# Optimization experiments

Hardware: AMD Instinct MI355X
Metric: run time of the kernel (lower is better)

Reference implementation:

```python
import jax, jax.numpy as jnp
import numpy as np

B, N, D, H = 4, 256, 32, 512

def setup_inputs() -> dict:
    key = jax.random.key(0)
    ks = jax.random.split(key, 6)
    z = jax.random.normal(ks[0], (B, N, D), dtype=jnp.float32)
    motif_mask = (jax.random.uniform(ks[1], (B, N)) > 0.5).astype(jnp.float32)
    residue_mask = jnp.ones((B, N), dtype=jnp.float32)
    # Linear weights stored as (in, out); scaled like torch default init
    W1 = jax.random.normal(ks[2], (D * D, H), dtype=jnp.float32) / np.sqrt(D * D)
    b1 = jnp.zeros((H,), dtype=jnp.float32)
    W2 = jax.random.normal(ks[3], (H, H // 2), dtype=jnp.float32) / np.sqrt(H)
    b2 = jnp.zeros((H // 2,), dtype=jnp.float32)
    W3 = jax.random.normal(ks[4], (H // 2, 1), dtype=jnp.float32) / np.sqrt(H // 2)
    b3 = jnp.zeros((1,), dtype=jnp.float32)
    return {"z": z, "motif_mask": motif_mask, "residue_mask": residue_mask,
            "W1": W1, "b1": b1, "W2": W2, "b2": b2, "W3": W3, "b3": b3}

def reference(z, motif_mask, residue_mask, W1, b1, W2, b2, W3, b3):
    # kron[b,i,j, a*D+c] = z[b,i,a] * z[b,j,c]; first Linear on kron is the
    # bilinear form z_i^T W1_h z_j -- compute via two matmuls, never
    # materializing the (B,N,N,D^2) tensor.
    d = z.shape[-1]
    W1r = W1.reshape(d, d, -1)                      # (D, D, H); axis0 = z_i dim, axis1 = z_j dim
    tmp = jnp.einsum('bia,ach->bihc', z, W1r)        # (B, N, H, D)
    h1 = jax.nn.relu(jnp.einsum('bihc,bjc->bijh', tmp, z) + b1)  # (B, N, N, H)
    h2 = jax.nn.relu(jnp.einsum('bijh,hk->bijk', h1, W2) + b2)   # (B, N, N, H/2)
    contact_logits = (jnp.einsum('bijk,ko->bijo', h2, W3) + b3)[..., 0]  # (B, N, N)
    outer_mask = motif_mask[:, None, :] * motif_mask[:, :, None]
    contact_logits = contact_logits * outer_mask
    contact_map = jax.nn.sigmoid(contact_logits)
    return (contact_map, contact_logits)
```

## Files before the change

### kernel.cpp

```cpp
#include <hip/hip_runtime.h>
#include <hip/hip_bf16.h>
#include <cstdint>
#include <cstddef>

#define NB 4
#define NN 256
#define DD 32
#define HH 512

typedef __attribute__((ext_vector_type(8))) short short8;
typedef __attribute__((ext_vector_type(4))) float f32x4;
typedef __attribute__((ext_vector_type(16))) float f32x16;

static __device__ __forceinline__ unsigned cvtpk(float a, float b) {
  unsigned r;
  asm("v_cvt_pk_bf16_f32 %0, %1, %2" : "=v"(r) : "v"(a), "v"(b));
  return r;
}
static __device__ __forceinline__ unsigned short f2bf1(float a) {
  return (unsigned short)(cvtpk(a, 0.f) & 0xffffu);
}

static __device__ __forceinline__ short8 pack8(float4 a0, float4 a1) {
  union { unsigned u[4]; short8 s; } r;
  r.u[0] = cvtpk(a0.x, a0.y); r.u[1] = cvtpk(a0.z, a0.w);
  r.u[2] = cvtpk(a1.x, a1.y); r.u[3] = cvtpk(a1.z, a1.w);
  return r.s;
}

__global__ __launch_bounds__(256) void prep0(const float* __restrict__ W1,
                                             unsigned short* __restrict__ W1F) {
  const int f = blockIdx.x * 256 + threadIdx.x;
  #pragma unroll
  for (int r = 0; r < 4; ++r) {
    int row = r * 16384 + f;
    int lane = row & 63;
    int nt = (row >> 6) & 7, w2 = (row >> 9) & 3, nblk = row >> 11;
    int quad = lane >> 4, l16 = lane & 15;
    int nl = w2 * 128 + l16 * 8 + nt;
    int hl = nl >> 5, c = nl & 31;
    const float* src = W1 + (size_t)(nblk * 16 + hl);
    float v[8];
    #pragma unroll
    for (int e = 0; e < 8; ++e)
      v[e] = src[(size_t)((quad * 8 + e) * 32 + c) * 512];
    uint4 p;
    p.x = cvtpk(v[0], v[1]); p.y = cvtpk(v[2], v[3]);
    p.z = cvtpk(v[4], v[5]); p.w = cvtpk(v[6], v[7]);
    *(uint4*)&W1F[(size_t)row * 8] = p;
  }
}

__global__ __launch_bounds__(256) void prep1(const float* __restrict__ z,
                                             const unsigned short* __restrict__ W1F,
                                             const float* __restrict__ W2,
                                             const float* __restrict__ motif,
                                             unsigned short* __restrict__ W2F,
                                             unsigned short* __restrict__ Tall,
                                             int* __restrict__ jlist,
                                             int* __restrict__ jcnt,
                                             int* __restrict__ wq,
                                             int* __restrict__ wqn,
                                             float* __restrict__ out) {
  const int blk = blockIdx.x;
  const int tid = threadIdx.x;
  if (blk < 512) {
    const int nblk = blk >> 4, mgrp = blk & 15;
    const int bibase = mgrp * 64;
    const int w2 = tid >> 6, lane = tid & 63;
    const int quad = lane >> 4, l16 = lane & 15;

    short8 bfr[8];
    #pragma unroll
    for (int nt = 0; nt < 8; ++nt)
      bfr[nt] = *(const short8*)&W1F[(size_t)((((nblk * 4 + w2) * 8) + nt) * 64 + lane) * 8];

    const int ncol = nblk * 512 + w2 * 128 + l16 * 8;
    #pragma unroll
    for (int mtg = 0; mtg < 2; ++mtg) {
      short8 afr[2];
      #pragma unroll
      for (int mi = 0; mi < 2; ++mi) {
        const float* zr = z + (size_t)(bibase + (mtg * 2 + mi) * 16 + l16) * 32 + quad * 8;
        float4 a0 = *(const float4*)(zr);
        float4 a1 = *(const float4*)(zr + 4);
        afr[mi] = pack8(a0, a1);
      }
      f32x4 d[2][8];
      #pragma unroll
      for (int mi = 0; mi < 2; ++mi)
        #pragma unroll
        for (int nt = 0; nt < 8; ++nt)
          d[mi][nt] = __builtin_amdgcn_mfma_f32_16x16x32_bf16(
              afr[mi], bfr[nt], (f32x4){0.f, 0.f, 0.f, 0.f}, 0, 0, 0);
      #pragma unroll
      for (int mi = 0; mi < 2; ++mi)
        #pragma unroll
        for (int r = 0; r < 4; ++r) {
          int rowbi = bibase + (mtg * 2 + mi) * 16 + quad * 4 + r;
          if (motif[rowbi] != 0.f) {
            uint4 p;
            p.x = cvtpk(d[mi][0][r], d[mi][1][r]);
            p.y = cvtpk(d[mi][2][r], d[mi][3][r]);
            p.z = cvtpk(d[mi][4][r], d[mi][5][r]);
            p.w = cvtpk(d[mi][6][r], d[mi][7][r]);
            *(uint4*)&Tall[(size_t)rowbi * 16384 + ncol] = p;
          }
        }
    }
  } else if (blk < 576) {
    int f8 = (blk - 512) * 256 + tid;
    int lane = f8 & 63;
    int nt = (f8 >> 6) & 1, s = (f8 >> 7) & 3, hc = (f8 >> 9) & 7, w = (f8 >> 12) & 3;
    int k2 = w * 64 + nt * 32 + (lane & 31);
    int hb = hc * 64 + s * 16 + (lane >> 5) * 8;
    float v[8];
    #pragma unroll
    for (int e = 0; e < 8; ++e) v[e] = W2[(hb + e) * 256 + k2];
    uint4 p;
    p.x = cvtpk(v[0], v[1]); p.y = cvtpk(v[2], v[3]);
    p.z = cvtpk(v[4], v[5]); p.w = cvtpk(v[6], v[7]);
    ((uint4*)W2F)[f8] = p;
  } else if (blk == 576) {
    __shared__ int itemc[4];
    __shared__ int baseh[4];
    const int w = tid >> 6, lane = tid & 63;
    int cnt = 0;
    if (w < NB) {
      #pragma unroll
      for (int ch = 0; ch < 4; ++ch) {
        int j = ch * 64 + lane;
        float m = motif[w * 256 + j];
        bool alive = (m != 0.f);
        unsigned long long mk = __ballot(alive);
        unsigned long long below = mk & ((1ull << lane) - 1ull);
        int pos = __popcll(below);
        if (alive) jlist[w * 256 + cnt + pos] = j;
        cnt += __popcll(mk);
      }
      if (lane == 0) {
        jcnt[w] = cnt;
        itemc[w] = cnt * ((cnt + 63) >> 6);
      }
    }
    __syncthreads();
    if (tid == 0) {
      int s = 0;
      #pragma unroll
      for (int k = 0; k < NB; ++k) { baseh[k] = s; s += itemc[k]; }
      *wqn = s;
    }
    __syncthreads();
    if (w < NB) {
      const int K = (cnt + 63) >> 6;
      const int base = baseh[w];
      const int L2n = cnt * K;
      int rank = 0;
      #pragma unroll
      for (int ch = 0; ch < 4; ++ch) {
        int i = ch * 64 + lane;
        bool alive = (motif[w * 256 + i] != 0.f);
        unsigned long long mk = __ballot(alive);
        unsigned long long below = mk & ((1ull << lane) - 1ull);
        int pos = __popcll(below);
        if (alive) {
          int idx0 = (rank + pos) * K;
          for (int jt = 0; jt < K; ++jt) {
            int idx = idx0 + jt;
            int nidx = idx;
            if (K == 2) {
              int g = idx >> 4;
              if (g * 16 + 16 <= L2n)
                nidx = g * 16 + ((idx & 1) << 3) + ((idx >> 1) & 7);
            }
            wq[base + nidx] = (w * 256 + i) * 4 + jt;
          }
        }
        rank += __popcll(mk);
      }
    }
  } else {
    const size_t OUT2 = (size_t)NB * NN * NN;
    const int c = blk - 577;
    for (int p = c * 4096 + tid; p < (c + 1) * 4096; p += 256) {
      int bi = p >> 8, j = p & 255, b = bi >> 8;
      if (motif[bi] == 0.f || motif[b * 256 + j] == 0.f) {
        out[p] = 0.5f;
        out[OUT2 + p] = 0.f;
      }
    }
  }
}

__global__ __launch_bounds__(256) void fused(const unsigned short* __restrict__ Tall,
                                             const unsigned short* __restrict__ W2F,
                                             const float* __restrict__ z,
                                             const float* __restrict__ b1,
                                             const float* __restrict__ b2,
                                             const float* __restrict__ W3,
                                             const float* __restrict__ b3,
                                             const float* __restrict__ motif,
                                             const int* __restrict__ jlist,
                                             const int* __restrict__ jcnt,
                                             const int* __restrict__ wq,
                                             const int* __restrict__ wqn,
                                             float* __restrict__ out) {
  __shared__ unsigned short h1s[2][64 * 264];
  __shared__ float red[256];

  const int bx = blockIdx.x;
  const int tid = threadIdx.x;
  const size_t OUT2 = (size_t)NB * NN * NN;
  const int nq = *wqn;

  if (bx >= nq) return;
  const int item = wq[bx];

  const int w = tid >> 6, lane = tid & 63;
  const int quad = lane >> 4, l16 = lane & 15;
  const int L = lane >> 5, c32 = lane & 31;

  const int bi = item >> 2, jt = item & 3;
  const int b = bi >> 8;
  const int cnt = jcnt[b];
  const int slotbase = jt * 64;
  const float mi_v = motif[bi];

  const unsigned short* Tbase = Tall + (size_t)bi * 16384 + (w * 16 + l16) * 32 + quad * 8;
  const unsigned short* Wp = W2F + w * 32768 + lane * 8;
  const float* b1base = b1 + w * 16 + quad * 4;

  short8 bfp[8][2];
  #pragma unroll
  for (int p = 0; p < 8; ++p) {
    bfp[p][0] = *(const short8*)(Wp + p * 1024);
    bfp[p][1] = *(const short8*)(Wp + p * 1024 + 512);
  }

  short8 zfr[4];
  #pragma unroll
  for (int sg = 0; sg < 4; ++sg) {
    int slot = slotbase + sg * 16 + l16;
    int sc = slot < cnt ? slot : cnt - 1;
    int jj = jlist[b * 256 + sc] & 255;
    const float* zr = z + (size_t)(b * 256 + jj) * 32 + quad * 8;
    float4 a0 = *(const float4*)(zr);
    float4 a1 = *(const float4*)(zr + 4);
    zfr[sg] = pack8(a0, a1);
  }

  float b2v[2], w3v[2];
  #pragma unroll
  for (int nt = 0; nt < 2; ++nt) {
    int k2 = w * 64 + nt * 32 + c32;
    b2v[nt] = b2[k2];
    w3v[nt] = W3[k2];
  }

  f32x16 acc[2][2];
  #pragma unroll
  for (int mt = 0; mt < 2; ++mt)
    #pragma unroll
    for (int nt = 0; nt < 2; ++nt)
      acc[mt][nt] = (f32x16){0.f,0.f,0.f,0.f,0.f,0.f,0.f,0.f,
                             0.f,0.f,0.f,0.f,0.f,0.f,0.f,0.f};

  short8 tfr[4];

  #pragma unroll
  for (int q = 0; q < 4; ++q)
    tfr[q] = *(const short8*)(Tbase + q * 2048);
  #pragma unroll
  for (int q = 0; q < 4; ++q) {
    float4 b1f = *(const float4*)(b1base + q * 64);
    f32x4 cin = {b1f.x, b1f.y, b1f.z, b1f.w};
    #pragma unroll
    for (int sg = 0; sg < 4; ++sg) {
      f32x4 d = __builtin_amdgcn_mfma_f32_16x16x32_bf16(tfr[q], zfr[sg], cin, 0, 0, 0);
      uint2 p;
      p.x = cvtpk(fmaxf(d[0], 0.f), fmaxf(d[1], 0.f));
      p.y = cvtpk(fmaxf(d[2], 0.f), fmaxf(d[3], 0.f));
      *(uint2*)&h1s[0][(sg * 16 + l16) * 264 + q * 64 + w * 16 + quad * 4] = p;
    }
  }
  __syncthreads();

  #pragma unroll
  for (int q = 0; q < 4; ++q)
    tfr[q] = *(const short8*)(Tbase + (4 + q) * 2048);
  #pragma unroll
  for (int q = 0; q < 4; ++q) {
    float4 b1f = *(const float4*)(b1base + (4 + q) * 64);
    f32x4 cin = {b1f.x, b1f.y, b1f.z, b1f.w};
    #pragma unroll
    for (int sg = 0; sg < 4; ++sg) {
      f32x4 d = __builtin_amdgcn_mfma_f32_16x16x32_bf16(tfr[q], zfr[sg], cin, 0, 0, 0);
      uint2 p;
      p.x = cvtpk(fmaxf(d[0], 0.f), fmaxf(d[1], 0.f));
      p.y = cvtpk(fmaxf(d[2], 0.f), fmaxf(d[3], 0.f));
      *(uint2*)&h1s[1][(sg * 16 + l16) * 264 + q * 64 + w * 16 + quad * 4] = p;
    }
  }
  {
    const unsigned short* Wh = Wp;
    const unsigned short* Wh1 = Wp + 16384;
    const unsigned short* h1r = &h1s[0][c32 * 264 + L * 8];
    short8 afp[2][2];
    afp[0][0] = *(const short8*)(h1r);
    afp[0][1] = *(const short8*)(h1r + 32 * 264);
    afp[1][0] = *(const short8*)(h1r + 16);
    afp[1][1] = *(const short8*)(h1r + 32 * 264 + 16);
    #pragma unroll
    for (int u = 0; u < 16; ++u) {
      const int cur = u & 1, bq = u & 7;
      short8 a0 = afp[cur][0], a1 = afp[cur][1];
      short8 b0 = bfp[bq][0], b1q = bfp[bq][1];
      if (u < 14) {
        afp[cur][0] = *(const short8*)(h1r + (u + 2) * 16);
        afp[cur][1] = *(const short8*)(h1r + 32 * 264 + (u + 2) * 16);
      }
      if (u < 8) {
        bfp[bq][0] = *(const short8*)(Wh + (u + 8) * 1024);
        bfp[bq][1] = *(const short8*)(Wh + (u + 8) * 1024 + 512);
      } else {
        bfp[bq][0] = *(const short8*)(Wh1 + (u - 8) * 1024);
        bfp[bq][1] = *(const short8*)(Wh1 + (u - 8) * 1024 + 512);
      }
      acc[0][0] = __builtin_amdgcn_mfma_f32_32x32x16_bf16(a0, b0, acc[0][0], 0, 0, 0);
      acc[0][1] = __builtin_amdgcn_mfma_f32_32x32x16_bf16(a0, b1q, acc[0][1], 0, 0, 0);
      acc[1][0] = __builtin_amdgcn_mfma_f32_32x32x16_bf16(a1, b0, acc[1][0], 0, 0, 0);
      acc[1][1] = __builtin_amdgcn_mfma_f32_32x32x16_bf16(a1, b1q, acc[1][1], 0, 0, 0);
    }
  }
  __syncthreads();

  {
    const unsigned short* Wh = Wp + 16384;
    const unsigned short* h1r = &h1s[1][c32 * 264 + L * 8];
    short8 afp[2][2];
    afp[0][0] = *(const short8*)(h1r);
    afp[0][1] = *(const short8*)(h1r + 32 * 264);
    afp[1][0] = *(const short8*)(h1r + 16);
    afp[1][1] = *(const short8*)(h1r + 32 * 264 + 16);
    #pragma unroll
    for (int u = 0; u < 16; ++u) {
      const int cur = u & 1, bq = u & 7;
      short8 a0 = afp[cur][0], a1 = afp[cur][1];
      short8 b0 = bfp[bq][0], b1q = bfp[bq][1];
      if (u < 14) {
        afp[cur][0] = *(const short8*)(h1r + (u + 2) * 16);
        afp[cur][1] = *(const short8*)(h1r + 32 * 264 + (u + 2) * 16);
      }
      if (u < 8) {
        bfp[bq][0] = *(const short8*)(Wh + (u + 8) * 1024);
        bfp[bq][1] = *(const short8*)(Wh + (u + 8) * 1024 + 512);
      }
      acc[0][0] = __builtin_amdgcn_mfma_f32_32x32x16_bf16(a0, b0, acc[0][0], 0, 0, 0);
      acc[0][1] = __builtin_amdgcn_mfma_f32_32x32x16_bf16(a0, b1q, acc[0][1], 0, 0, 0);
      acc[1][0] = __builtin_amdgcn_mfma_f32_32x32x16_bf16(a1, b0, acc[1][0], 0, 0, 0);
      acc[1][1] = __builtin_amdgcn_mfma_f32_32x32x16_bf16(a1, b1q, acc[1][1], 0, 0, 0);
    }
  }

  float pr[2][16];
  #pragma unroll
  for (int mt = 0; mt < 2; ++mt)
    #pragma unroll
    for (int reg = 0; reg < 16; ++reg) {
      float s = 0.f;
      #pragma unroll
      for (int nt = 0; nt < 2; ++nt) {
        float v = acc[mt][nt][reg] + b2v[nt];
        v = v > 0.f ? v : 0.f;
        s += v * w3v[nt];
      }
      s += __shfl_xor(s, 1);
      s += __shfl_xor(s, 2);
      s += __shfl_xor(s, 4);
      s += __shfl_xor(s, 8);
      s += __shfl_xor(s, 16);
      pr[mt][reg] = s;
    }
  if (c32 == 0) {
    #pragma unroll
    for (int mt = 0; mt < 2; ++mt)
      #pragma unroll
      for (int g = 0; g < 4; ++g) {
        float4 vv = {pr[mt][g * 4 + 0], pr[mt][g * 4 + 1],
                     pr[mt][g * 4 + 2], pr[mt][g * 4 + 3]};
        *(float4*)&red[w * 64 + mt * 32 + g * 8 + L * 4] = vv;
      }
  }
  __syncthreads();
  if (tid < 64) {
    int slot = slotbase + tid;
    if (slot < cnt) {
      int j = jlist[b * 256 + slot] & 255;
      float logit = red[tid] + red[64 + tid] + red[128 + tid] + red[192 + tid] + b3[0];
      float mm = mi_v * motif[b * 256 + j];
      logit *= mm;
      float map = 1.f / (1.f + expf(-logit));
      size_t idx = (size_t)bi * 256 + j;
      out[idx] = map;
      out[OUT2 + idx] = logit;
    }
  }
}

extern "C" void kernel_launch(void* const* d_in, const int* in_sizes, int n_in,
                              void* d_out, int out_size, void* d_ws, size_t ws_size,
                              hipStream_t stream) {
  const float* z     = (const float*)d_in[0];
  const float* motif = (const float*)d_in[1];
  const float* W1 = (const float*)d_in[3];
  const float* b1 = (const float*)d_in[4];
  const float* W2 = (const float*)d_in[5];
  const float* b2 = (const float*)d_in[6];
  const float* W3 = (const float*)d_in[7];
  const float* b3 = (const float*)d_in[8];
  float* out = (float*)d_out;

  char* ws = (char*)d_ws;
  unsigned short* Tall = (unsigned short*)ws;
  unsigned short* W2F  = (unsigned short*)(ws + 33554432);
  unsigned short* W1F  = (unsigned short*)(ws + 33554432 + 262144);
  char* tail = ws + 33554432 + 262144 + 1048576;
  int* jlist = (int*)(tail);
  int* jcnt  = (int*)(tail + 4096);
  int* wq    = (int*)(tail + 4096 + 64);
  int* wqn   = (int*)(tail + 4096 + 64 + 16384);

  prep0<<<64, 256, 0, stream>>>(W1, W1F);
  prep1<<<641, 256, 0, stream>>>(z, W1F, W2, motif, W2F, Tall,
                                 jlist, jcnt, wq, wqn, out);
  fused<<<4096, 256, 0, stream>>>(Tall, W2F, z, b1, b2, W3, b3, motif,
                                  jlist, jcnt, wq, wqn, out);
}
```

Before: 123.7 us.

## Make fused kernel persistent and overlap next item's layer-1 with current layer-2

```diff
diff --git a/kernel.cpp b/kernel.cpp
--- a/kernel.cpp
+++ b/kernel.cpp
@@ -7,6 +7,7 @@
 #define NN 256
 #define DD 32
 #define HH 512
+#define FGRID 512
 
 typedef __attribute__((ext_vector_type(8))) short short8;
 typedef __attribute__((ext_vector_type(4))) float f32x4;
@@ -214,40 +215,13 @@
   const int nq = *wqn;
 
   if (bx >= nq) return;
-  const int item = wq[bx];
 
   const int w = tid >> 6, lane = tid & 63;
   const int quad = lane >> 4, l16 = lane & 15;
   const int L = lane >> 5, c32 = lane & 31;
 
-  const int bi = item >> 2, jt = item & 3;
-  const int b = bi >> 8;
-  const int cnt = jcnt[b];
-  const int slotbase = jt * 64;
-  const float mi_v = motif[bi];
-
-  const unsigned short* Tbase = Tall + (size_t)bi * 16384 + (w * 16 + l16) * 32 + quad * 8;
   const unsigned short* Wp = W2F + w * 32768 + lane * 8;
   const float* b1base = b1 + w * 16 + quad * 4;
-
-  short8 bfp[8][2];
-  #pragma unroll
-  for (int p = 0; p < 8; ++p) {
-    bfp[p][0] = *(const short8*)(Wp + p * 1024);
-    bfp[p][1] = *(const short8*)(Wp + p * 1024 + 512);
-  }
-
-  short8 zfr[4];
-  #pragma unroll
-  for (int sg = 0; sg < 4; ++sg) {
-    int slot = slotbase + sg * 16 + l16;
-    int sc = slot < cnt ? slot : cnt - 1;
-    int jj = jlist[b * 256 + sc] & 255;
-    const float* zr = z + (size_t)(b * 256 + jj) * 32 + quad * 8;
-    float4 a0 = *(const float4*)(zr);
-    float4 a1 = *(const float4*)(zr + 4);
-    zfr[sg] = pack8(a0, a1);
-  }
 
   float b2v[2], w3v[2];
   #pragma unroll
@@ -256,6 +230,33 @@
     b2v[nt] = b2[k2];
     w3v[nt] = W3[k2];
   }
+  const float b3s = b3[0];
+
+  short8 bfp[8][2];
+  #pragma unroll
+  for (int p = 0; p < 8; ++p) {
+    bfp[p][0] = *(const short8*)(Wp + p * 1024);
+    bfp[p][1] = *(const short8*)(Wp + p * 1024 + 512);
+  }
+
+  int item = wq[bx];
+  int bi = item >> 2, jt = item & 3;
+  int cnt = jcnt[bi >> 8];
+  int slotbase = jt * 64;
+  float mi_v = motif[bi];
+  const unsigned short* Tbase = Tall + (size_t)bi * 16384 + (w * 16 + l16) * 32 + quad * 8;
+
+  short8 zfr[4];
+  #pragma unroll
+  for (int sg = 0; sg < 4; ++sg) {
+    int slot = slotbase + sg * 16 + l16;
+    int sc = slot < cnt ? slot : cnt - 1;
+    int jj = jlist[(bi >> 8) * 256 + sc] & 255;
+    const float* zr = z + (size_t)((bi >> 8) * 256 + jj) * 32 + quad * 8;
+    float4 a0 = *(const float4*)(zr);
+    float4 a1 = *(const float4*)(zr + 4);
+    zfr[sg] = pack8(a0, a1);
+  }
 
   f32x16 acc[2][2];
   #pragma unroll
@@ -265,145 +266,210 @@
       acc[mt][nt] = (f32x16){0.f,0.f,0.f,0.f,0.f,0.f,0.f,0.f,
                              0.f,0.f,0.f,0.f,0.f,0.f,0.f,0.f};
 
-  short8 tfr[4];
-
-  #pragma unroll
-  for (int q = 0; q < 4; ++q)
-    tfr[q] = *(const short8*)(Tbase + q * 2048);
-  #pragma unroll
-  for (int q = 0; q < 4; ++q) {
-    float4 b1f = *(const float4*)(b1base + q * 64);
-    f32x4 cin = {b1f.x, b1f.y, b1f.z, b1f.w};
-    #pragma unroll
-    for (int sg = 0; sg < 4; ++sg) {
-      f32x4 d = __builtin_amdgcn_mfma_f32_16x16x32_bf16(tfr[q], zfr[sg], cin, 0, 0, 0);
-      uint2 p;
-      p.x = cvtpk(fmaxf(d[0], 0.f), fmaxf(d[1], 0.f));
-      p.y = cvtpk(fmaxf(d[2], 0.f), fmaxf(d[3], 0.f));
-      *(uint2*)&h1s[0][(sg * 16 + l16) * 264 + q * 64 + w * 16 + quad * 4] = p;
+  {
+    short8 tfr[4];
+    #pragma unroll
+    for (int q = 0; q < 4; ++q)
+      tfr[q] = *(const short8*)(Tbase + q * 2048);
+    #pragma unroll
+    for (int q = 0; q < 4; ++q) {
+      float4 b1f = *(const float4*)(b1base + q * 64);
+      f32x4 cin = {b1f.x, b1f.y, b1f.z, b1f.w};
+      #pragma unroll
+      for (int sg = 0; sg < 4; ++sg) {
+        f32x4 d = __builtin_amdgcn_mfma_f32_16x16x32_bf16(tfr[q], zfr[sg], cin, 0, 0, 0);
+        uint2 p;
+        p.x = cvtpk(fmaxf(d[0], 0.f), fmaxf(d[1], 0.f));
+        p.y = cvtpk(fmaxf(d[2], 0.f), fmaxf(d[3], 0.f));
+        *(uint2*)&h1s[0][(sg * 16 + l16) * 264 + q * 64 + w * 16 + quad * 4] = p;
+      }
     }
   }
   __syncthreads();
 
-  #pragma unroll
-  for (int q = 0; q < 4; ++q)
-    tfr[q] = *(const short8*)(Tbase + (4 + q) * 2048);
-  #pragma unroll
-  for (int q = 0; q < 4; ++q) {
-    float4 b1f = *(const float4*)(b1base + (4 + q) * 64);
-    f32x4 cin = {b1f.x, b1f.y, b1f.z, b1f.w};
-    #pragma unroll
-    for (int sg = 0; sg < 4; ++sg) {
-      f32x4 d = __builtin_amdgcn_mfma_f32_16x16x32_bf16(tfr[q], zfr[sg], cin, 0, 0, 0);
-      uint2 p;
-      p.x = cvtpk(fmaxf(d[0], 0.f), fmaxf(d[1], 0.f));
-      p.y = cvtpk(fmaxf(d[2], 0.f), fmaxf(d[3], 0.f));
-      *(uint2*)&h1s[1][(sg * 16 + l16) * 264 + q * 64 + w * 16 + quad * 4] = p;
-    }
-  }
-  {
-    const unsigned short* Wh = Wp;
-    const unsigned short* Wh1 = Wp + 16384;
-    const unsigned short* h1r = &h1s[0][c32 * 264 + L * 8];
-    short8 afp[2][2];
-    afp[0][0] = *(const short8*)(h1r);
-    afp[0][1] = *(const short8*)(h1r + 32 * 264);
-    afp[1][0] = *(const short8*)(h1r + 16);
-    afp[1][1] = *(const short8*)(h1r + 32 * 264 + 16);
-    #pragma unroll
-    for (int u = 0; u < 16; ++u) {
-      const int cur = u & 1, bq = u & 7;
-      short8 a0 = afp[cur][0], a1 = afp[cur][1];
-      short8 b0 = bfp[bq][0], b1q = bfp[bq][1];
-      if (u < 14) {
-        afp[cur][0] = *(const short8*)(h1r + (u + 2) * 16);
-        afp[cur][1] = *(const short8*)(h1r + 32 * 264 + (u + 2) * 16);
-      }
-      if (u < 8) {
-        bfp[bq][0] = *(const short8*)(Wh + (u + 8) * 1024);
-        bfp[bq][1] = *(const short8*)(Wh + (u + 8) * 1024 + 512);
-      } else {
-        bfp[bq][0] = *(const short8*)(Wh1 + (u - 8) * 1024);
-        bfp[bq][1] = *(const short8*)(Wh1 + (u - 8) * 1024 + 512);
-      }
-      acc[0][0] = __builtin_amdgcn_mfma_f32_32x32x16_bf16(a0, b0, acc[0][0], 0, 0, 0);
-      acc[0][1] = __builtin_amdgcn_mfma_f32_32x32x16_bf16(a0, b1q, acc[0][1], 0, 0, 0);
-      acc[1][0] = __builtin_amdgcn_mfma_f32_32x32x16_bf16(a1, b0, acc[1][0], 0, 0, 0);
-      acc[1][1] = __builtin_amdgcn_mfma_f32_32x32x16_bf16(a1, b1q, acc[1][1], 0, 0, 0);
-    }
-  }
-  __syncthreads();
-
-  {
-    const unsigned short* Wh = Wp + 16384;
-    const unsigned short* h1r = &h1s[1][c32 * 264 + L * 8];
-    short8 afp[2][2];
-    afp[0][0] = *(const short8*)(h1r);
-    afp[0][1] = *(const short8*)(h1r + 32 * 264);
-    afp[1][0] = *(const short8*)(h1r + 16);
-    afp[1][1] = *(const short8*)(h1r + 32 * 264 + 16);
-    #pragma unroll
-    for (int u = 0; u < 16; ++u) {
-      const int cur = u & 1, bq = u & 7;
-      short8 a0 = afp[cur][0], a1 = afp[cur][1];
-      short8 b0 = bfp[bq][0], b1q = bfp[bq][1];
-      if (u < 14) {
-        afp[cur][0] = *(const short8*)(h1r + (u + 2) * 16);
-        afp[cur][1] = *(const short8*)(h1r + 32 * 264 + (u + 2) * 16);
-      }
-      if (u < 8) {
-        bfp[bq][0] = *(const short8*)(Wh + (u + 8) * 1024);
-        bfp[bq][1] = *(const short8*)(Wh + (u + 8) * 1024 + 512);
-      }
-      acc[0][0] = __builtin_amdgcn_mfma_f32_32x32x16_bf16(a0, b0, acc[0][0], 0, 0, 0);
-      acc[0][1] = __builtin_amdgcn_mfma_f32_32x32x16_bf16(a0, b1q, acc[0][1], 0, 0, 0);
-      acc[1][0] = __builtin_amdgcn_mfma_f32_32x32x16_bf16(a1, b0, acc[1][0], 0, 0, 0);
-      acc[1][1] = __builtin_amdgcn_mfma_f32_32x32x16_bf16(a1, b1q, acc[1][1], 0, 0, 0);
-    }
-  }
-
-  float pr[2][16];
-  #pragma unroll
-  for (int mt = 0; mt < 2; ++mt)
-    #pragma unroll
-    for (int reg = 0; reg < 16; ++reg) {
-      float s = 0.f;
-      #pragma unroll
-      for (int nt = 0; nt < 2; ++nt) {
-        float v = acc[mt][nt][reg] + b2v[nt];
-        v = v > 0.f ? v : 0.f;
-        s += v * w3v[nt];
-      }
-      s += __shfl_xor(s, 1);
-      s += __shfl_xor(s, 2);
-      s += __shfl_xor(s, 4);
-      s += __shfl_xor(s, 8);
-      s += __shfl_xor(s, 16);
-      pr[mt][reg] = s;
-    }
-  if (c32 == 0) {
+  #pragma unroll 1
+  for (int it = bx; it < nq; ) {
+    {
+      short8 tfr[4];
+      #pragma unroll
+      for (int q = 0; q < 4; ++q)
+        tfr[q] = *(const short8*)(Tbase + (4 + q) * 2048);
+      #pragma unroll
+      for (int q = 0; q < 4; ++q) {
+        float4 b1f = *(const float4*)(b1base + (4 + q) * 64);
+        f32x4 cin = {b1f.x, b1f.y, b1f.z, b1f.w};
+        #pragma unroll
+        for (int sg = 0; sg < 4; ++sg) {
+          f32x4 d = __builtin_amdgcn_mfma_f32_16x16x32_bf16(tfr[q], zfr[sg], cin, 0, 0, 0);
+          uint2 p;
+          p.x = cvtpk(fmaxf(d[0], 0.f), fmaxf(d[1], 0.f));
+          p.y = cvtpk(fmaxf(d[2], 0.f), fmaxf(d[3], 0.f));
+          *(uint2*)&h1s[1][(sg * 16 + l16) * 264 + q * 64 + w * 16 + quad * 4] = p;
+        }
+      }
+      const unsigned short* Wh = Wp;
+      const unsigned short* Wh1 = Wp + 16384;
+      const unsigned short* h1r = &h1s[0][c32 * 264 + L * 8];
+      short8 afp[2][2];
+      afp[0][0] = *(const short8*)(h1r);
+      afp[0][1] = *(const short8*)(h1r + 32 * 264);
+      afp[1][0] = *(const short8*)(h1r + 16);
+      afp[1][1] = *(const short8*)(h1r + 32 * 264 + 16);
+      #pragma unroll
+      for (int u = 0; u < 16; ++u) {
+        const int cur = u & 1, bq = u & 7;
+        short8 a0 = afp[cur][0], a1 = afp[cur][1];
+        short8 b0 = bfp[bq][0], b1q = bfp[bq][1];
+        if (u < 14) {
+          afp[cur][0] = *(const short8*)(h1r + (u + 2) * 16);
+          afp[cur][1] = *(const short8*)(h1r + 32 * 264 + (u + 2) * 16);
+        }
+        if (u < 8) {
+          bfp[bq][0] = *(const short8*)(Wh + (u + 8) * 1024);
+          bfp[bq][1] = *(const short8*)(Wh + (u + 8) * 1024 + 512);
+        } else {
+          bfp[bq][0] = *(const short8*)(Wh1 + (u - 8) * 1024);
+          bfp[bq][1] = *(const short8*)(Wh1 + (u - 8) * 1024 + 512);
+        }
+        acc[0][0] = __builtin_amdgcn_mfma_f32_32x32x16_bf16(a0, b0, acc[0][0], 0, 0, 0);
+        acc[0][1] = __builtin_amdgcn_mfma_f32_32x32x16_bf16(a0, b1q, acc[0][1], 0, 0, 0);
+        acc[1][0] = __builtin_amdgcn_mfma_f32_32x32x16_bf16(a1, b0, acc[1][0], 0, 0, 0);
+        acc[1][1] = __builtin_amdgcn_mfma_f32_32x32x16_bf16(a1, b1q, acc[1][1], 0, 0, 0);
+      }
+    }
+    __syncthreads();
+
+    const int nit = it + FGRID;
+    const bool hn = nit < nq;
+    int nbi = 0, nslotbase = 0, ncnt = 0;
+    float nmi = 0.f;
+    const unsigned short* nTbase = Tbase;
+    short8 nzfr[4];
+    if (hn) {
+      int nitem = wq[nit];
+      nbi = nitem >> 2;
+      int njt = nitem & 3;
+      ncnt = jcnt[nbi >> 8];
+      nslotbase = njt * 64;
+      nmi = motif[nbi];
+      nTbase = Tall + (size_t)nbi * 16384 + (w * 16 + l16) * 32 + quad * 8;
+      #pragma unroll
+      for (int sg = 0; sg < 4; ++sg) {
+        int slot = nslotbase + sg * 16 + l16;
+        int sc = slot < ncnt ? slot : ncnt - 1;
+        int jj = jlist[(nbi >> 8) * 256 + sc] & 255;
+        const float* zr = z + (size_t)((nbi >> 8) * 256 + jj) * 32 + quad * 8;
+        float4 a0 = *(const float4*)(zr);
+        float4 a1 = *(const float4*)(zr + 4);
+        nzfr[sg] = pack8(a0, a1);
+      }
+      short8 tfr[4];
+      #pragma unroll
+      for (int q = 0; q < 4; ++q)
+        tfr[q] = *(const short8*)(nTbase + q * 2048);
+      #pragma unroll
+      for (int q = 0; q < 4; ++q) {
+        float4 b1f = *(const float4*)(b1base + q * 64);
+        f32x4 cin = {b1f.x, b1f.y, b1f.z, b1f.w};
+        #pragma unroll
+        for (int sg = 0; sg < 4; ++sg) {
+          f32x4 d = __builtin_amdgcn_mfma_f32_16x16x32_bf16(tfr[q], nzfr[sg], cin, 0, 0, 0);
+          uint2 p;
+          p.x = cvtpk(fmaxf(d[0], 0.f), fmaxf(d[1], 0.f));
+          p.y = cvtpk(fmaxf(d[2], 0.f), fmaxf(d[3], 0.f));
+          *(uint2*)&h1s[0][(sg * 16 + l16) * 264 + q * 64 + w * 16 + quad * 4] = p;
+        }
+      }
+    }
+    {
+      const unsigned short* Wh = Wp + 16384;
+      const unsigned short* Wh0 = Wp;
+      const unsigned short* h1r = &h1s[1][c32 * 264 + L * 8];
+      short8 afp[2][2];
+      afp[0][0] = *(const short8*)(h1r);
+      afp[0][1] = *(const short8*)(h1r + 32 * 264);
+      afp[1][0] = *(const short8*)(h1r + 16);
+      afp[1][1] = *(const short8*)(h1r + 32 * 264 + 16);
+      #pragma unroll
+      for (int u = 0; u < 16; ++u) {
+        const int cur = u & 1, bq = u & 7;
+        short8 a0 = afp[cur][0], a1 = afp[cur][1];
+        short8 b0 = bfp[bq][0], b1q = bfp[bq][1];
+        if (u < 14) {
+          afp[cur][0] = *(const short8*)(h1r + (u + 2) * 16);
+          afp[cur][1] = *(const short8*)(h1r + 32 * 264 + (u + 2) * 16);
+        }
+        if (u < 8) {
+          bfp[bq][0] = *(const short8*)(Wh + (u + 8) * 1024);
+          bfp[bq][1] = *(const short8*)(Wh + (u + 8) * 1024 + 512);
+        } else {
+          bfp[bq][0] = *(const short8*)(Wh0 + (u - 8) * 1024);
+          bfp[bq][1] = *(const short8*)(Wh0 + (u - 8) * 1024 + 512);
+        }
+        acc[0][0] = __builtin_amdgcn_mfma_f32_32x32x16_bf16(a0, b0, acc[0][0], 0, 0, 0);
+        acc[0][1] = __builtin_amdgcn_mfma_f32_32x32x16_bf16(a0, b1q, acc[0][1], 0, 0, 0);
+        acc[1][0] = __builtin_amdgcn_mfma_f32_32x32x16_bf16(a1, b0, acc[1][0], 0, 0, 0);
+        acc[1][1] = __builtin_amdgcn_mfma_f32_32x32x16_bf16(a1, b1q, acc[1][1], 0, 0, 0);
+      }
+    }
+    {
+      float pr[2][16];
+      #pragma unroll
+      for (int mt = 0; mt < 2; ++mt)
+        #pragma unroll
+        for (int reg = 0; reg < 16; ++reg) {
+          float s = 0.f;
+          #pragma unroll
+          for (int nt = 0; nt < 2; ++nt) {
+            float v = acc[mt][nt][reg] + b2v[nt];
+            v = v > 0.f ? v : 0.f;
+            s += v * w3v[nt];
+          }
+          s += __shfl_xor(s, 1);
+          s += __shfl_xor(s, 2);
+          s += __shfl_xor(s, 4);
+          s += __shfl_xor(s, 8);
+          s += __shfl_xor(s, 16);
+          pr[mt][reg] = s;
+        }
+      if (c32 == 0) {
+        #pragma unroll
+        for (int mt = 0; mt < 2; ++mt)
+          #pragma unroll
+          for (int g = 0; g < 4; ++g) {
+            float4 vv = {pr[mt][g * 4 + 0], pr[mt][g * 4 + 1],
+                         pr[mt][g * 4 + 2], pr[mt][g * 4 + 3]};
+            *(float4*)&red[w * 64 + mt * 32 + g * 8 + L * 4] = vv;
+          }
+      }
+    }
+    __syncthreads();
+
+    if (tid < 64) {
+      int slot = slotbase + tid;
+      if (slot < cnt) {
+        int j = jlist[(bi >> 8) * 256 + slot] & 255;
+        float logit = red[tid] + red[64 + tid] + red[128 + tid] + red[192 + tid] + b3s;
+        float mm = mi_v * motif[(bi >> 8) * 256 + j];
+        logit *= mm;
+        float map = 1.f / (1.f + expf(-logit));
+        size_t idx = (size_t)bi * 256 + j;
+        out[idx] = map;
+        out[OUT2 + idx] = logit;
+      }
+    }
+
+    it = nit;
+    if (!hn) break;
+    bi = nbi; slotbase = nslotbase; cnt = ncnt; mi_v = nmi; Tbase = nTbase;
+    #pragma unroll
+    for (int sg = 0; sg < 4; ++sg) zfr[sg] = nzfr[sg];
     #pragma unroll
     for (int mt = 0; mt < 2; ++mt)
       #pragma unroll
-      for (int g = 0; g < 4; ++g) {
-        float4 vv = {pr[mt][g * 4 + 0], pr[mt][g * 4 + 1],
-                     pr[mt][g * 4 + 2], pr[mt][g * 4 + 3]};
-        *(float4*)&red[w * 64 + mt * 32 + g * 8 + L * 4] = vv;
-      }
-  }
-  __syncthreads();
-  if (tid < 64) {
-    int slot = slotbase + tid;
-    if (slot < cnt) {
-      int j = jlist[b * 256 + slot] & 255;
-      float logit = red[tid] + red[64 + tid] + red[128 + tid] + red[192 + tid] + b3[0];
-      float mm = mi_v * motif[b * 256 + j];
-      logit *= mm;
-      float map = 1.f / (1.f + expf(-logit));
-      size_t idx = (size_t)bi * 256 + j;
-      out[idx] = map;
-      out[OUT2 + idx] = logit;
-    }
+      for (int nt = 0; nt < 2; ++nt)
+        acc[mt][nt] = (f32x16){0.f,0.f,0.f,0.f,0.f,0.f,0.f,0.f,
+                               0.f,0.f,0.f,0.f,0.f,0.f,0.f,0.f};
   }
 }
 
@@ -433,6 +499,6 @@
   prep0<<<64, 256, 0, stream>>>(W1, W1F);
   prep1<<<641, 256, 0, stream>>>(z, W1F, W2, motif, W2F, Tall,
                                  jlist, jcnt, wq, wqn, out);
-  fused<<<4096, 256, 0, stream>>>(Tall, W2F, z, b1, b2, W3, b3, motif,
-                                  jlist, jcnt, wq, wqn, out);
-}
+  fused<<<FGRID, 256, 0, stream>>>(Tall, W2F, z, b1, b2, W3, b3, motif,
+                                   jlist, jcnt, wq, wqn, out);
+}
```

Result: slower. 142.8 us (+15.4%).
